# Optimization experiments

Measured on AMD Instinct MI355X. Metric: run time of the kernel, lower is better.

The kernel has to match this reference:

```python
import math
import jax, jax.numpy as jnp
import numpy as np

DIM = 128
NUM_PROJ = 256
ENC = jnp.asarray(2 ** np.arange(8), dtype=jnp.uint8)  # [1,2,4,...,128]
DEQUANT_SCALE = math.sqrt(math.pi / 2) / NUM_PROJ


def quantize_packed(x, S):
    # x: (..., dim) float32 -> packed uint8 (..., ceil(num_proj/8))
    projected = jnp.einsum('...d,pd->...p', x, S)
    signs = projected > 0  # bool (..., num_proj)
    pad_len = (-NUM_PROJ) % 8
    if pad_len > 0:
        pad = [(0, 0)] * (signs.ndim - 1) + [(0, pad_len)]
        signs = jnp.pad(signs, pad, constant_values=False)
    signs = signs.reshape(*signs.shape[:-1], -1, 8)  # (..., nbytes, 8)
    packed = jnp.sum(signs.astype(jnp.uint8) * ENC, axis=-1, dtype=jnp.uint8)
    return packed


def unpack_signs(packed):
    # packed: uint8 (..., nbytes) -> {-1,+1} float32 (..., num_proj)
    bits = jnp.bitwise_and(packed[..., None], ENC) > 0  # (..., nbytes, 8)
    bits = bits.reshape(*packed.shape[:-1], -1)[..., :NUM_PROJ]
    return bits.astype(jnp.float32) * 2.0 - 1.0


def setup_inputs() -> dict:
    key = jax.random.key(0)
    k1, k2, k3 = jax.random.split(key, 3)
    query = jax.random.normal(k1, (2, 32, 4096, DIM), dtype=jnp.float32)
    key_t = jax.random.normal(k2, (2, 32, 4096, DIM), dtype=jnp.float32)
    S = jax.random.normal(k3, (NUM_PROJ, DIM), dtype=jnp.float32)
    return {"query": query, "key": key_t, "S": S}


def reference(query, key, S):
    # quantize keys to bit-packed sign sketch, then estimate <query, key>
    packed = quantize_packed(key, S)                       # uint8 (..., 32)
    signs = unpack_signs(packed)                           # (..., 256)
    q_proj = jnp.einsum('...d,pd->...p', query, S)         # (..., 256)
    est = DEQUANT_SCALE * jnp.sum(q_proj * signs, axis=-1) # (B,H,S)
    return est
```

## Files before the change

### kernel.cpp

```cpp
#include <hip/hip_runtime.h>
#include <stdint.h>

#define NPROJ 256
#define DIM 128
#define MT 64
#define PCHUNK 32
#define NCHUNK (NPROJ / PCHUNK)
#define LSTR 136
#define TAU 2.0e-3f
#define QCAP 512
#define DEQ 0.004895758348888673f

typedef __attribute__((ext_vector_type(8))) short bf16x8;
typedef __attribute__((ext_vector_type(4))) float f32x4;

__device__ __forceinline__ ushort f2bf(float x) {
    union { float f; uint32_t u; } v; v.f = x;
    uint32_t r = v.u + 0x7FFFu + ((v.u >> 16) & 1u);
    return (ushort)(r >> 16);
}
__device__ __forceinline__ float bf2f(ushort h) {
    union { float f; uint32_t u; } v; v.u = ((uint32_t)h) << 16;
    return v.f;
}

__global__ __launch_bounds__(256, 2) void qjl_main(
    const float* __restrict__ qg, const float* __restrict__ kg,
    const float* __restrict__ Sg, float* __restrict__ out)
{
    __shared__ ushort kh[MT * LSTR];
    __shared__ ushort kl[MT * LSTR];
    __shared__ ushort qh[MT * LSTR];
    __shared__ ushort sh[PCHUNK * LSTR];
    __shared__ ushort sl[PCHUNK * LSTR];
    __shared__ float  est_s[MT];
    __shared__ uint32_t qmeta[QCAP];
    __shared__ float    qdlt[QCAP];
    __shared__ int      qn;

    const int tid  = threadIdx.x;
    const int lane = tid & 63;
    const int wv   = tid >> 6;
    const long tok0 = (long)blockIdx.x * MT;

    if (tid == 0) qn = 0;

    {
        const float4* k4 = (const float4*)(kg + tok0 * DIM);
        const float4* q4 = (const float4*)(qg + tok0 * DIM);
        #pragma unroll
        for (int i = 0; i < 8; i++) {
            int f = tid + i * 256;
            int row = f >> 5, c4 = f & 31;
            int off = row * LSTR + c4 * 4;
            float4 kv = k4[f];
            ushort h0 = f2bf(kv.x), h1 = f2bf(kv.y), h2 = f2bf(kv.z), h3 = f2bf(kv.w);
            kh[off + 0] = h0; kh[off + 1] = h1; kh[off + 2] = h2; kh[off + 3] = h3;
            kl[off + 0] = f2bf(kv.x - bf2f(h0));
            kl[off + 1] = f2bf(kv.y - bf2f(h1));
            kl[off + 2] = f2bf(kv.z - bf2f(h2));
            kl[off + 3] = f2bf(kv.w - bf2f(h3));
            float4 qv = q4[f];
            qh[off + 0] = f2bf(qv.x); qh[off + 1] = f2bf(qv.y);
            qh[off + 2] = f2bf(qv.z); qh[off + 3] = f2bf(qv.w);
        }
    }

    float est[4] = {0.f, 0.f, 0.f, 0.f};
    const int arow = wv * 16 + (lane & 15);
    const int kq   = (lane >> 4) * 8;
    const int brow = lane & 15;

    for (int c = 0; c < NCHUNK; c++) {
        if (c) __syncthreads();
        {
            const float4* s4 = (const float4*)(Sg + (long)c * PCHUNK * DIM);
            #pragma unroll
            for (int i = 0; i < 4; i++) {
                int f = tid + i * 256;
                int row = f >> 5, c4 = f & 31;
                int off = row * LSTR + c4 * 4;
                float4 sv = s4[f];
                ushort h0 = f2bf(sv.x), h1 = f2bf(sv.y), h2 = f2bf(sv.z), h3 = f2bf(sv.w);
                sh[off + 0] = h0; sh[off + 1] = h1; sh[off + 2] = h2; sh[off + 3] = h3;
                sl[off + 0] = f2bf(sv.x - bf2f(h0));
                sl[off + 1] = f2bf(sv.y - bf2f(h1));
                sl[off + 2] = f2bf(sv.z - bf2f(h2));
                sl[off + 3] = f2bf(sv.w - bf2f(h3));
            }
        }
        __syncthreads();

        f32x4 kacc0 = {0,0,0,0}, kacc1 = {0,0,0,0};
        f32x4 qacc0 = {0,0,0,0}, qacc1 = {0,0,0,0};
        #pragma unroll
        for (int ks = 0; ks < 4; ks++) {
            int acol = ks * 32 + kq;
            bf16x8 akh = *(const bf16x8*)&kh[arow * LSTR + acol];
            bf16x8 akl = *(const bf16x8*)&kl[arow * LSTR + acol];
            bf16x8 aqh = *(const bf16x8*)&qh[arow * LSTR + acol];
            bf16x8 b0h = *(const bf16x8*)&sh[brow * LSTR + acol];
            bf16x8 b0l = *(const bf16x8*)&sl[brow * LSTR + acol];
            bf16x8 b1h = *(const bf16x8*)&sh[(brow + 16) * LSTR + acol];
            bf16x8 b1l = *(const bf16x8*)&sl[(brow + 16) * LSTR + acol];
            kacc0 = __builtin_amdgcn_mfma_f32_16x16x32_bf16(akh, b0h, kacc0, 0, 0, 0);
            kacc0 = __builtin_amdgcn_mfma_f32_16x16x32_bf16(akl, b0h, kacc0, 0, 0, 0);
            kacc0 = __builtin_amdgcn_mfma_f32_16x16x32_bf16(akh, b0l, kacc0, 0, 0, 0);
            qacc0 = __builtin_amdgcn_mfma_f32_16x16x32_bf16(aqh, b0h, qacc0, 0, 0, 0);
            kacc1 = __builtin_amdgcn_mfma_f32_16x16x32_bf16(akh, b1h, kacc1, 0, 0, 0);
            kacc1 = __builtin_amdgcn_mfma_f32_16x16x32_bf16(akl, b1h, kacc1, 0, 0, 0);
            kacc1 = __builtin_amdgcn_mfma_f32_16x16x32_bf16(akh, b1l, kacc1, 0, 0, 0);
            qacc1 = __builtin_amdgcn_mfma_f32_16x16x32_bf16(aqh, b1h, qacc1, 0, 0, 0);
        }

        #pragma unroll
        for (int r = 0; r < 4; r++) {
            int tl = wv * 16 + (lane >> 4) * 4 + r;
            float kv = kacc0[r], qv = qacc0[r];
            float s = (kv > 0.f) ? 1.f : -1.f;
            est[r] += qv * s;
            if (fabsf(kv) < TAU) {
                int p = c * PCHUNK + (lane & 15);
                int idx = atomicAdd(&qn, 1);
                if (idx < QCAP) {
                    qmeta[idx] = (uint32_t)tl | ((uint32_t)p << 8) | ((kv > 0.f ? 1u : 0u) << 16);
                    qdlt[idx]  = DEQ * qv * s;
                }
            }
            kv = kacc1[r]; qv = qacc1[r];
            s = (kv > 0.f) ? 1.f : -1.f;
            est[r] += qv * s;
            if (fabsf(kv) < TAU) {
                int p = c * PCHUNK + 16 + (lane & 15);
                int idx = atomicAdd(&qn, 1);
                if (idx < QCAP) {
                    qmeta[idx] = (uint32_t)tl | ((uint32_t)p << 8) | ((kv > 0.f ? 1u : 0u) << 16);
                    qdlt[idx]  = DEQ * qv * s;
                }
            }
        }
    }

    #pragma unroll
    for (int r = 0; r < 4; r++) {
        float e = est[r];
        e += __shfl_xor(e, 1);
        e += __shfl_xor(e, 2);
        e += __shfl_xor(e, 4);
        e += __shfl_xor(e, 8);
        if ((lane & 15) == 0) est_s[wv * 16 + (lane >> 4) * 4 + r] = DEQ * e;
    }
    __syncthreads();

    int nc = qn < QCAP ? qn : QCAP;
    for (int i = wv; i < nc; i += 4) {
        uint32_t m = qmeta[i];
        int tl = m & 255;
        int p  = (m >> 8) & 255;
        int sf = (m >> 16) & 1;
        const float2* kr = (const float2*)(kg + (tok0 + tl) * DIM);
        const float2* sr = (const float2*)(Sg + (long)p * DIM);
        float2 ka = kr[lane], sa = sr[lane];
        double acc = (double)ka.x * (double)sa.x + (double)ka.y * (double)sa.y;
        acc += __shfl_xor(acc, 1);
        acc += __shfl_xor(acc, 2);
        acc += __shfl_xor(acc, 4);
        acc += __shfl_xor(acc, 8);
        acc += __shfl_xor(acc, 16);
        acc += __shfl_xor(acc, 32);
        int st = (acc > 0.0) ? 1 : 0;
        if (lane == 0 && st != sf) atomicAdd(&est_s[tl], -2.f * qdlt[i]);
    }
    __syncthreads();

    if (tid < MT) out[tok0 + tid] = est_s[tid];
}

extern "C" void kernel_launch(void* const* d_in, const int* in_sizes, int n_in,
                              void* d_out, int out_size, void* d_ws, size_t ws_size,
                              hipStream_t stream) {
    const float* q = (const float*)d_in[0];
    const float* k = (const float*)d_in[1];
    const float* S = (const float*)d_in[2];
    float* out = (float*)d_out;
    int nblocks = out_size / MT;
    hipLaunchKernelGGL(qjl_main, dim3(nblocks), dim3(256), 0, stream, q, k, S, out);
}
```

Baseline: 357.9 us.

## Switch to fp16 single-pass MFMA with pre-swizzled S and register-resident operands

Replaces the bf16 hi/lo split (three MFMAs per key projection) with a single fp16 MFMA, widening the near-zero recheck threshold so the exact fp64 fallback covers the larger fp16 error. A small prep kernel converts S once into a fragment-ordered fp16 layout in workspace, so the main kernel reads B fragments straight from global memory and drops all LDS staging and per-chunk barriers. Query and key fragments are loaded directly into registers, each block now handles 128 tokens, and occupancy is raised to 3 blocks per CU. The cost is more tokens entering the recheck queue, with a risk of overflowing QCAP and losing correctness, plus an extra kernel launch.

```diff
diff --git a/kernel.cpp b/kernel.cpp
--- a/kernel.cpp
+++ b/kernel.cpp
@@ -1,163 +1,139 @@
 #include <hip/hip_runtime.h>
 #include <stdint.h>
 
+#define DIM 128
 #define NPROJ 256
-#define DIM 128
-#define MT 64
-#define PCHUNK 32
-#define NCHUNK (NPROJ / PCHUNK)
-#define LSTR 136
-#define TAU 2.0e-3f
+#define TPB 128
+#define TAU 0.035f
 #define QCAP 512
 #define DEQ 0.004895758348888673f
 
-typedef __attribute__((ext_vector_type(8))) short bf16x8;
-typedef __attribute__((ext_vector_type(4))) float f32x4;
+typedef _Float16 f16x8 __attribute__((ext_vector_type(8)));
+typedef float f32x4 __attribute__((ext_vector_type(4)));
 
-__device__ __forceinline__ ushort f2bf(float x) {
-    union { float f; uint32_t u; } v; v.f = x;
-    uint32_t r = v.u + 0x7FFFu + ((v.u >> 16) & 1u);
-    return (ushort)(r >> 16);
-}
-__device__ __forceinline__ float bf2f(ushort h) {
-    union { float f; uint32_t u; } v; v.u = ((uint32_t)h) << 16;
-    return v.f;
+__global__ __launch_bounds__(256) void qjl_prep(const float* __restrict__ Sg,
+                                                _Float16* __restrict__ ws) {
+    int t = blockIdx.x * 256 + threadIdx.x;
+    int lane = t & 63, fid = t >> 6;
+    int f = fid & 1, ks = (fid >> 1) & 3, c = fid >> 3;
+    int p = c * 32 + f * 16 + (lane & 15);
+    int d0 = ks * 32 + (lane >> 4) * 8;
+    const float4* s4 = (const float4*)(Sg + p * DIM + d0);
+    float4 a = s4[0], b = s4[1];
+    f16x8 h = {(_Float16)a.x, (_Float16)a.y, (_Float16)a.z, (_Float16)a.w,
+               (_Float16)b.x, (_Float16)b.y, (_Float16)b.z, (_Float16)b.w};
+    *(f16x8*)(ws + (size_t)fid * 512 + lane * 8) = h;
 }
 
-__global__ __launch_bounds__(256, 2) void qjl_main(
+__global__ __launch_bounds__(256, 3) void qjl_main(
     const float* __restrict__ qg, const float* __restrict__ kg,
-    const float* __restrict__ Sg, float* __restrict__ out)
+    const float* __restrict__ Sg, const _Float16* __restrict__ ws,
+    float* __restrict__ out)
 {
-    __shared__ ushort kh[MT * LSTR];
-    __shared__ ushort kl[MT * LSTR];
-    __shared__ ushort qh[MT * LSTR];
-    __shared__ ushort sh[PCHUNK * LSTR];
-    __shared__ ushort sl[PCHUNK * LSTR];
-    __shared__ float  est_s[MT];
+    __shared__ float    est_s[TPB];
     __shared__ uint32_t qmeta[QCAP];
     __shared__ float    qdlt[QCAP];
     __shared__ int      qn;
 
-    const int tid  = threadIdx.x;
-    const int lane = tid & 63;
-    const int wv   = tid >> 6;
-    const long tok0 = (long)blockIdx.x * MT;
+    const int tid = threadIdx.x, lane = tid & 63, wv = tid >> 6;
+    const int m = lane & 15, quad = lane >> 4;
+    const long tok0 = (long)blockIdx.x * TPB;
+    if (tid == 0) qn = 0;
+    __syncthreads();
 
-    if (tid == 0) qn = 0;
-
-    {
-        const float4* k4 = (const float4*)(kg + tok0 * DIM);
-        const float4* q4 = (const float4*)(qg + tok0 * DIM);
+    f16x8 ak[2][4], aq[2][4];
+    #pragma unroll
+    for (int rb = 0; rb < 2; ++rb) {
+        long row = tok0 + wv * 32 + rb * 16 + m;
+        const float* kr = kg + row * DIM;
+        const float* qr = qg + row * DIM;
         #pragma unroll
-        for (int i = 0; i < 8; i++) {
-            int f = tid + i * 256;
-            int row = f >> 5, c4 = f & 31;
-            int off = row * LSTR + c4 * 4;
-            float4 kv = k4[f];
-            ushort h0 = f2bf(kv.x), h1 = f2bf(kv.y), h2 = f2bf(kv.z), h3 = f2bf(kv.w);
-            kh[off + 0] = h0; kh[off + 1] = h1; kh[off + 2] = h2; kh[off + 3] = h3;
-            kl[off + 0] = f2bf(kv.x - bf2f(h0));
-            kl[off + 1] = f2bf(kv.y - bf2f(h1));
-            kl[off + 2] = f2bf(kv.z - bf2f(h2));
-            kl[off + 3] = f2bf(kv.w - bf2f(h3));
-            float4 qv = q4[f];
-            qh[off + 0] = f2bf(qv.x); qh[off + 1] = f2bf(qv.y);
-            qh[off + 2] = f2bf(qv.z); qh[off + 3] = f2bf(qv.w);
+        for (int ks = 0; ks < 4; ++ks) {
+            int d0 = ks * 32 + quad * 8;
+            float4 x = *(const float4*)(kr + d0);
+            float4 y = *(const float4*)(kr + d0 + 4);
+            ak[rb][ks] = (f16x8){(_Float16)x.x, (_Float16)x.y, (_Float16)x.z, (_Float16)x.w,
+                                 (_Float16)y.x, (_Float16)y.y, (_Float16)y.z, (_Float16)y.w};
+            float4 u = *(const float4*)(qr + d0);
+            float4 v = *(const float4*)(qr + d0 + 4);
+            aq[rb][ks] = (f16x8){(_Float16)u.x, (_Float16)u.y, (_Float16)u.z, (_Float16)u.w,
+                                 (_Float16)v.x, (_Float16)v.y, (_Float16)v.z, (_Float16)v.w};
         }
     }
 
-    float est[4] = {0.f, 0.f, 0.f, 0.f};
-    const int arow = wv * 16 + (lane & 15);
-    const int kq   = (lane >> 4) * 8;
-    const int brow = lane & 15;
+    float est[8] = {0.f, 0.f, 0.f, 0.f, 0.f, 0.f, 0.f, 0.f};
 
-    for (int c = 0; c < NCHUNK; c++) {
-        if (c) __syncthreads();
-        {
-            const float4* s4 = (const float4*)(Sg + (long)c * PCHUNK * DIM);
+    for (int c = 0; c < 8; ++c) {
+        f16x8 b0[4], b1[4];
+        #pragma unroll
+        for (int ks = 0; ks < 4; ++ks) {
+            b0[ks] = *(const f16x8*)(ws + (size_t)(c * 8 + ks * 2 + 0) * 512 + lane * 8);
+            b1[ks] = *(const f16x8*)(ws + (size_t)(c * 8 + ks * 2 + 1) * 512 + lane * 8);
+        }
+        #pragma unroll
+        for (int rb = 0; rb < 2; ++rb) {
+            f32x4 kacc0 = {0,0,0,0}, kacc1 = {0,0,0,0};
+            f32x4 qacc0 = {0,0,0,0}, qacc1 = {0,0,0,0};
             #pragma unroll
-            for (int i = 0; i < 4; i++) {
-                int f = tid + i * 256;
-                int row = f >> 5, c4 = f & 31;
-                int off = row * LSTR + c4 * 4;
-                float4 sv = s4[f];
-                ushort h0 = f2bf(sv.x), h1 = f2bf(sv.y), h2 = f2bf(sv.z), h3 = f2bf(sv.w);
-                sh[off + 0] = h0; sh[off + 1] = h1; sh[off + 2] = h2; sh[off + 3] = h3;
-                sl[off + 0] = f2bf(sv.x - bf2f(h0));
-                sl[off + 1] = f2bf(sv.y - bf2f(h1));
-                sl[off + 2] = f2bf(sv.z - bf2f(h2));
-                sl[off + 3] = f2bf(sv.w - bf2f(h3));
+            for (int ks = 0; ks < 4; ++ks) {
+                kacc0 = __builtin_amdgcn_mfma_f32_16x16x32_f16(ak[rb][ks], b0[ks], kacc0, 0, 0, 0);
+                kacc1 = __builtin_amdgcn_mfma_f32_16x16x32_f16(ak[rb][ks], b1[ks], kacc1, 0, 0, 0);
+                qacc0 = __builtin_amdgcn_mfma_f32_16x16x32_f16(aq[rb][ks], b0[ks], qacc0, 0, 0, 0);
+                qacc1 = __builtin_amdgcn_mfma_f32_16x16x32_f16(aq[rb][ks], b1[ks], qacc1, 0, 0, 0);
             }
-        }
-        __syncthreads();
-
-        f32x4 kacc0 = {0,0,0,0}, kacc1 = {0,0,0,0};
-        f32x4 qacc0 = {0,0,0,0}, qacc1 = {0,0,0,0};
-        #pragma unroll
-        for (int ks = 0; ks < 4; ks++) {
-            int acol = ks * 32 + kq;
-            bf16x8 akh = *(const bf16x8*)&kh[arow * LSTR + acol];
-            bf16x8 akl = *(const bf16x8*)&kl[arow * LSTR + acol];
-            bf16x8 aqh = *(const bf16x8*)&qh[arow * LSTR + acol];
-            bf16x8 b0h = *(const bf16x8*)&sh[brow * LSTR + acol];
-            bf16x8 b0l = *(const bf16x8*)&sl[brow * LSTR + acol];
-            bf16x8 b1h = *(const bf16x8*)&sh[(brow + 16) * LSTR + acol];
-            bf16x8 b1l = *(const bf16x8*)&sl[(brow + 16) * LSTR + acol];
-            kacc0 = __builtin_amdgcn_mfma_f32_16x16x32_bf16(akh, b0h, kacc0, 0, 0, 0);
-            kacc0 = __builtin_amdgcn_mfma_f32_16x16x32_bf16(akl, b0h, kacc0, 0, 0, 0);
-            kacc0 = __builtin_amdgcn_mfma_f32_16x16x32_bf16(akh, b0l, kacc0, 0, 0, 0);
-            qacc0 = __builtin_amdgcn_mfma_f32_16x16x32_bf16(aqh, b0h, qacc0, 0, 0, 0);
-            kacc1 = __builtin_amdgcn_mfma_f32_16x16x32_bf16(akh, b1h, kacc1, 0, 0, 0);
-            kacc1 = __builtin_amdgcn_mfma_f32_16x16x32_bf16(akl, b1h, kacc1, 0, 0, 0);
-            kacc1 = __builtin_amdgcn_mfma_f32_16x16x32_bf16(akh, b1l, kacc1, 0, 0, 0);
-            qacc1 = __builtin_amdgcn_mfma_f32_16x16x32_bf16(aqh, b1h, qacc1, 0, 0, 0);
-        }
-
-        #pragma unroll
-        for (int r = 0; r < 4; r++) {
-            int tl = wv * 16 + (lane >> 4) * 4 + r;
-            float kv = kacc0[r], qv = qacc0[r];
-            float s = (kv > 0.f) ? 1.f : -1.f;
-            est[r] += qv * s;
-            if (fabsf(kv) < TAU) {
-                int p = c * PCHUNK + (lane & 15);
-                int idx = atomicAdd(&qn, 1);
-                if (idx < QCAP) {
-                    qmeta[idx] = (uint32_t)tl | ((uint32_t)p << 8) | ((kv > 0.f ? 1u : 0u) << 16);
-                    qdlt[idx]  = DEQ * qv * s;
+            #pragma unroll
+            for (int r = 0; r < 4; ++r) {
+                int tl = wv * 32 + rb * 16 + quad * 4 + r;
+                {
+                    float kv = kacc0[r], qv = qacc0[r];
+                    float sg = (kv > 0.f) ? 1.f : -1.f;
+                    est[rb * 4 + r] += qv * sg;
+                    if (fabsf(kv) < TAU) {
+                        int p = c * 32 + m;
+                        int idx = atomicAdd(&qn, 1);
+                        if (idx < QCAP) {
+                            qmeta[idx] = (uint32_t)tl | ((uint32_t)p << 8) | ((kv > 0.f ? 1u : 0u) << 16);
+                            qdlt[idx]  = DEQ * qv * sg;
+                        }
+                    }
                 }
-            }
-            kv = kacc1[r]; qv = qacc1[r];
-            s = (kv > 0.f) ? 1.f : -1.f;
-            est[r] += qv * s;
-            if (fabsf(kv) < TAU) {
-                int p = c * PCHUNK + 16 + (lane & 15);
-                int idx = atomicAdd(&qn, 1);
-                if (idx < QCAP) {
-                    qmeta[idx] = (uint32_t)tl | ((uint32_t)p << 8) | ((kv > 0.f ? 1u : 0u) << 16);
-                    qdlt[idx]  = DEQ * qv * s;
+                {
+                    float kv = kacc1[r], qv = qacc1[r];
+                    float sg = (kv > 0.f) ? 1.f : -1.f;
+                    est[rb * 4 + r] += qv * sg;
+                    if (fabsf(kv) < TAU) {
+                        int p = c * 32 + 16 + m;
+                        int idx = atomicAdd(&qn, 1);
+                        if (idx < QCAP) {
+                            qmeta[idx] = (uint32_t)tl | ((uint32_t)p << 8) | ((kv > 0.f ? 1u : 0u) << 16);
+                            qdlt[idx]  = DEQ * qv * sg;
+                        }
+                    }
                 }
             }
         }
     }
 
     #pragma unroll
-    for (int r = 0; r < 4; r++) {
-        float e = est[r];
-        e += __shfl_xor(e, 1);
-        e += __shfl_xor(e, 2);
-        e += __shfl_xor(e, 4);
-        e += __shfl_xor(e, 8);
-        if ((lane & 15) == 0) est_s[wv * 16 + (lane >> 4) * 4 + r] = DEQ * e;
+    for (int rb = 0; rb < 2; ++rb) {
+        #pragma unroll
+        for (int r = 0; r < 4; ++r) {
+            float e = est[rb * 4 + r];
+            e += __shfl_xor(e, 1);
+            e += __shfl_xor(e, 2);
+            e += __shfl_xor(e, 4);
+            e += __shfl_xor(e, 8);
+            if (m == 0) est_s[wv * 32 + rb * 16 + quad * 4 + r] = DEQ * e;
+        }
     }
     __syncthreads();
 
     int nc = qn < QCAP ? qn : QCAP;
     for (int i = wv; i < nc; i += 4) {
-        uint32_t m = qmeta[i];
-        int tl = m & 255;
-        int p  = (m >> 8) & 255;
-        int sf = (m >> 16) & 1;
+        uint32_t mm = qmeta[i];
+        int tl = mm & 255;
+        int p  = (mm >> 8) & 255;
+        int sf = (mm >> 16) & 1;
         const float2* kr = (const float2*)(kg + (tok0 + tl) * DIM);
         const float2* sr = (const float2*)(Sg + (long)p * DIM);
         float2 ka = kr[lane], sa = sr[lane];
@@ -173,7 +149,7 @@
     }
     __syncthreads();
 
-    if (tid < MT) out[tok0 + tid] = est_s[tid];
+    if (tid < TPB) out[tok0 + tid] = est_s[tid];
 }
 
 extern "C" void kernel_launch(void* const* d_in, const int* in_sizes, int n_in,
@@ -183,6 +159,8 @@
     const float* k = (const float*)d_in[1];
     const float* S = (const float*)d_in[2];
     float* out = (float*)d_out;
-    int nblocks = out_size / MT;
-    hipLaunchKernelGGL(qjl_main, dim3(nblocks), dim3(256), 0, stream, q, k, S, out);
+    _Float16* ws = (_Float16*)d_ws;
+    hipLaunchKernelGGL(qjl_prep, dim3(16), dim3(256), 0, stream, S, ws);
+    int nblocks = out_size / TPB;
+    hipLaunchKernelGGL(qjl_main, dim3(nblocks), dim3(256), 0, stream, q, k, S, ws, out);
 }
```

After: 346.5 us. 1.03x faster.
